# Optimization experiments

Measured on AMD Instinct MI355X. Metric: run time of the kernel, lower is better.

## Reference

```python
import jax, jax.numpy as jnp
import numpy as np

Q_MAX = 127.0  # int8 symmetric quant range
EPS = 1e-7

def setup_inputs() -> dict:
    key = jax.random.key(0)
    k1, k2, k3, k4 = jax.random.split(key, 4)
    M, K, N = 8192, 4096, 4096
    x = jax.random.normal(k1, (M, K), dtype=jnp.float32)
    # int8 weight stored as int32 for portability; values in [-127, 127]
    weight_i8 = jax.random.randint(k2, (N, K), -127, 128, dtype=jnp.int32)
    # per-output-channel weight scale (small positive)
    w_scale = jax.random.uniform(k3, (N,), dtype=jnp.float32) * 0.01 + 1e-4
    bias = jax.random.normal(k4, (N,), dtype=jnp.float32)
    return {"x": x, "weight_i8": weight_i8, "w_scale": w_scale, "bias": bias}

def reference(x, weight_i8, w_scale, bias):
    # per-token dynamic symmetric quantization of activations
    absmax = jnp.max(jnp.abs(x), axis=-1, keepdims=True)            # [M, 1]
    x_scale = jnp.maximum(absmax, EPS) / Q_MAX                       # [M, 1]
    x_q = jnp.clip(jnp.round(x / x_scale), -Q_MAX, Q_MAX)            # [M, K] int values in fp32
    acc = jnp.einsum('mk,nk->mn', x_q, weight_i8.astype(jnp.float32))  # [M, N]
    out = acc * x_scale * w_scale[None, :] + bias[None, :]
    return out
```

## Files before the change

### kernel.cpp

```cpp
#include <hip/hip_runtime.h>
#include <stdint.h>

#define Q_MAX_F 127.0f
#define EPS_F 1e-7f

typedef int   v4i __attribute__((ext_vector_type(4)));
typedef float v4f __attribute__((ext_vector_type(4)));

__global__ __launch_bounds__(256) void quant_x_kernel(
    const float* __restrict__ x, int8_t* __restrict__ xq,
    float* __restrict__ xscale, int K) {
  const int row = blockIdx.x;
  const int t = threadIdx.x;
  const float* xr = x + (size_t)row * K;

  float v[16];
  float m = 0.f;
#pragma unroll
  for (int c = 0; c < 4; ++c) {
    v4f f = *(const v4f*)(xr + c * 1024 + t * 4);
#pragma unroll
    for (int j = 0; j < 4; ++j) {
      v[c * 4 + j] = f[j];
      m = fmaxf(m, fabsf(f[j]));
    }
  }
#pragma unroll
  for (int off = 32; off; off >>= 1) m = fmaxf(m, __shfl_xor(m, off));
  __shared__ float sm[4];
  if ((t & 63) == 0) sm[t >> 6] = m;
  __syncthreads();
  m = fmaxf(fmaxf(sm[0], sm[1]), fmaxf(sm[2], sm[3]));

  const float s = fmaxf(m, EPS_F) / Q_MAX_F;
  const float inv = 1.0f / s;
  if (t == 0) xscale[row] = s;

  int* xqi = (int*)xq;
#pragma unroll
  for (int c = 0; c < 4; ++c) {
    int packed = 0;
#pragma unroll
    for (int j = 0; j < 4; ++j) {
      float q = rintf(v[c * 4 + j] * inv);
      q = fminf(fmaxf(q, -127.f), 127.f);
      packed |= ((int)q & 0xff) << (8 * j);
    }
    xqi[(size_t)row * (K / 4) + c * 256 + t] = packed;
  }
}

__global__ __launch_bounds__(256) void pack_w_kernel(
    const int* __restrict__ w, int8_t* __restrict__ wq, long n4) {
  long i = (long)blockIdx.x * 256 + threadIdx.x;
  if (i >= n4) return;
  v4i a = ((const v4i*)w)[i];
  int packed = (a[0] & 0xff) | ((a[1] & 0xff) << 8) |
               ((a[2] & 0xff) << 16) | ((a[3] & 0xff) << 24);
  ((int*)wq)[i] = packed;
}

#define BM 256
#define BN 256

__global__ __launch_bounds__(512, 2) void w8a8_gemm_kernel(
    const int8_t* __restrict__ xq, const int8_t* __restrict__ wq,
    const float* __restrict__ xscale, const float* __restrict__ wscale,
    const float* __restrict__ bias, float* __restrict__ out,
    int M, int N, int K) {
  extern __shared__ char lds[];

  const int t = threadIdx.x;
  const int lane = t & 63;
  const int wid = t >> 6;
  const int wr = wid >> 2;
  const int wc = wid & 3;

  const int nwg = gridDim.x;
  int bid = blockIdx.x;
  int wg = ((nwg & 7) == 0) ? ((bid & 7) * (nwg >> 3) + (bid >> 3)) : bid;

  const int nbn = N / BN;
  const int bm = (wg / nbn) * BM;
  const int bn = (wg % nbn) * BN;

  const char* gA = (const char*)xq + (size_t)bm * K;
  const char* gB = (const char*)wq + (size_t)bn * K;

  v4i acc[8][4] = {};

  auto stage_part = [&](int kt, int p) {
    const char* gsrc = p ? gB : gA;
    char* dstbase = lds + (size_t)(kt & 3) * 32768 + p * 16384;
#pragma unroll
    for (int i = 0; i < 2; ++i) {
      const int lin = i * 8192 + wid * 1024 + lane * 16;
      const int row = lin >> 6;
      const int cs = (lane & 3) ^ ((row >> 1) & 3);
      const char* src = gsrc + (size_t)row * K + kt * 64 + cs * 16;
      __builtin_amdgcn_global_load_lds(
          (const __attribute__((address_space(1))) void*)src,
          (__attribute__((address_space(3))) void*)(dstbase + i * 8192 + wid * 1024),
          16, 0, 0);
    }
  };

  const int NT = K / 64;
  const int rl = lane & 15;
  const int ck = lane >> 4;

  for (int kt = 0; kt < 3; ++kt) { stage_part(kt, 0); stage_part(kt, 1); }
  asm volatile("s_waitcnt vmcnt(8)" ::: "memory");
  asm volatile("s_barrier" ::: "memory");

  for (int kt = 0; kt < NT; ++kt) {
    const char* bufA = lds + (size_t)(kt & 3) * 32768;
    const char* bufB = bufA + 16384;

    v4i b[4], a[4];
#pragma unroll
    for (int j = 0; j < 4; ++j) {
      const int r = wc * 64 + j * 16 + rl;
      b[j] = *(const v4i*)(bufB + r * 64 + ((ck ^ ((r >> 1) & 3)) << 4));
    }
#pragma unroll
    for (int i = 0; i < 4; ++i) {
      const int r = wr * 128 + i * 16 + rl;
      a[i] = *(const v4i*)(bufA + r * 64 + ((ck ^ ((r >> 1) & 3)) << 4));
    }
    if (kt + 3 < NT) stage_part(kt + 3, 0);
    __builtin_amdgcn_s_setprio(1);
#pragma unroll
    for (int i = 0; i < 4; ++i)
#pragma unroll
      for (int j = 0; j < 4; ++j)
        acc[i][j] = __builtin_amdgcn_mfma_i32_16x16x64_i8(a[i], b[j], acc[i][j], 0, 0, 0);
    __builtin_amdgcn_s_setprio(0);
    asm volatile("s_barrier" ::: "memory");

#pragma unroll
    for (int i = 0; i < 4; ++i) {
      const int r = wr * 128 + 64 + i * 16 + rl;
      a[i] = *(const v4i*)(bufA + r * 64 + ((ck ^ ((r >> 1) & 3)) << 4));
    }
    if (kt + 3 < NT) stage_part(kt + 3, 1);
    __builtin_amdgcn_s_setprio(1);
#pragma unroll
    for (int i = 0; i < 4; ++i)
#pragma unroll
      for (int j = 0; j < 4; ++j)
        acc[4 + i][j] = __builtin_amdgcn_mfma_i32_16x16x64_i8(a[i], b[j], acc[4 + i][j], 0, 0, 0);
    __builtin_amdgcn_s_setprio(0);

    if (kt <= NT - 4)      asm volatile("s_waitcnt vmcnt(8)" ::: "memory");
    else if (kt == NT - 3) asm volatile("s_waitcnt vmcnt(4)" ::: "memory");
    else if (kt == NT - 2) asm volatile("s_waitcnt vmcnt(0)" ::: "memory");
    asm volatile("s_barrier" ::: "memory");
  }

  const int r0 = (lane >> 4) * 4;
  const int cn = lane & 15;
#pragma unroll
  for (int i = 0; i < 8; ++i) {
    const int growb = bm + wr * 128 + i * 16 + r0;
#pragma unroll
    for (int j = 0; j < 4; ++j) {
      const int gcol = bn + wc * 64 + j * 16 + cn;
      const float wsc = wscale[gcol];
      const float bs = bias[gcol];
#pragma unroll
      for (int r = 0; r < 4; ++r) {
        const int grow = growb + r;
        const float xs = xscale[grow];
        out[(size_t)grow * N + gcol] = (float)acc[i][j][r] * (xs * wsc) + bs;
      }
    }
  }
}

extern "C" void kernel_launch(void* const* d_in, const int* in_sizes, int n_in,
                              void* d_out, int out_size, void* d_ws, size_t ws_size,
                              hipStream_t stream) {
  const float* x = (const float*)d_in[0];
  const int* w = (const int*)d_in[1];
  const float* wscale = (const float*)d_in[2];
  const float* bias = (const float*)d_in[3];
  float* out = (float*)d_out;

  const int N = in_sizes[2];
  const long wk = (long)in_sizes[1];
  const int K = (int)(wk / N);
  const int M = (int)((long)in_sizes[0] / K);

  int8_t* xq = (int8_t*)d_ws;
  int8_t* wq = xq + (size_t)M * K;
  float* xscale = (float*)(wq + (size_t)N * K);

  quant_x_kernel<<<M, 256, 0, stream>>>(x, xq, xscale, K);

  const long n4 = (long)N * K / 4;
  pack_w_kernel<<<(int)((n4 + 255) / 256), 256, 0, stream>>>(w, wq, n4);

  const int nwg = (M / BM) * (N / BN);
  w8a8_gemm_kernel<<<nwg, 512, 131072, stream>>>(xq, wq, xscale, wscale, bias,
                                                 out, M, N, K);
}
```

Before: 398.7 us.

## Switch GEMM to 32x32x32 int8 MFMA and fuse quant/pack prep kernels

The GEMM inner loop moves from 16x16x64 to 32x32x32 int8 MFMA tiles. Both A and B stages are issued at the start of each k-step, and the mid-iteration barrier is dropped. The activation quantization and weight packing kernels are merged into one launch that splits its blocks between the two jobs with grid-stride loops, and each thread now writes one 16-byte vector per row. This aims to cut launch overhead, halve LDS fragment reads per MFMA and give larger MFMA ops, at the cost of a new epilogue layout and less overlap between LDS reads and staging.

```diff
diff --git a/kernel.cpp b/kernel.cpp
--- a/kernel.cpp
+++ b/kernel.cpp
@@ -4,60 +4,62 @@
 #define Q_MAX_F 127.0f
 #define EPS_F 1e-7f
 
-typedef int   v4i __attribute__((ext_vector_type(4)));
-typedef float v4f __attribute__((ext_vector_type(4)));
-
-__global__ __launch_bounds__(256) void quant_x_kernel(
+typedef int   v4i  __attribute__((ext_vector_type(4)));
+typedef int   v16i __attribute__((ext_vector_type(16)));
+typedef float v4f  __attribute__((ext_vector_type(4)));
+
+__global__ __launch_bounds__(256) void prep_kernel(
     const float* __restrict__ x, int8_t* __restrict__ xq,
-    float* __restrict__ xscale, int K) {
-  const int row = blockIdx.x;
+    float* __restrict__ xscale,
+    const int* __restrict__ w, int8_t* __restrict__ wq,
+    int M, int K, long n4, int QB) {
   const int t = threadIdx.x;
-  const float* xr = x + (size_t)row * K;
-
-  float v[16];
-  float m = 0.f;
-#pragma unroll
-  for (int c = 0; c < 4; ++c) {
-    v4f f = *(const v4f*)(xr + c * 1024 + t * 4);
-#pragma unroll
-    for (int j = 0; j < 4; ++j) {
-      v[c * 4 + j] = f[j];
-      m = fmaxf(m, fabsf(f[j]));
+  if ((int)blockIdx.x < QB) {
+    __shared__ float sm[4];
+    for (int row = blockIdx.x; row < M; row += QB) {
+      const float* xr = x + (size_t)row * K + t * 16;
+      float v[16];
+      float m = 0.f;
+#pragma unroll
+      for (int c = 0; c < 4; ++c) {
+        v4f f = *(const v4f*)(xr + c * 4);
+#pragma unroll
+        for (int j = 0; j < 4; ++j) {
+          v[c * 4 + j] = f[j];
+          m = fmaxf(m, fabsf(f[j]));
+        }
+      }
+#pragma unroll
+      for (int off = 32; off; off >>= 1) m = fmaxf(m, __shfl_xor(m, off));
+      if ((t & 63) == 0) sm[t >> 6] = m;
+      __syncthreads();
+      m = fmaxf(fmaxf(sm[0], sm[1]), fmaxf(sm[2], sm[3]));
+      __syncthreads();
+      const float s = fmaxf(m, EPS_F) / Q_MAX_F;
+      const float inv = 1.0f / s;
+      if (t == 0) xscale[row] = s;
+      v4i pk;
+#pragma unroll
+      for (int c = 0; c < 4; ++c) {
+        int pw = 0;
+#pragma unroll
+        for (int j = 0; j < 4; ++j) {
+          float q = rintf(v[c * 4 + j] * inv);
+          q = fminf(fmaxf(q, -127.f), 127.f);
+          pw |= ((int)q & 0xff) << (8 * j);
+        }
+        pk[c] = pw;
+      }
+      *(v4i*)(xq + (size_t)row * K + t * 16) = pk;
+    }
+  } else {
+    const long stride = (long)(gridDim.x - QB) * 256;
+    for (long i = (long)((int)blockIdx.x - QB) * 256 + t; i < n4; i += stride) {
+      v4i a = ((const v4i*)w)[i];
+      ((int*)wq)[i] = (a[0] & 0xff) | ((a[1] & 0xff) << 8) |
+                      ((a[2] & 0xff) << 16) | ((a[3] & 0xff) << 24);
     }
   }
-#pragma unroll
-  for (int off = 32; off; off >>= 1) m = fmaxf(m, __shfl_xor(m, off));
-  __shared__ float sm[4];
-  if ((t & 63) == 0) sm[t >> 6] = m;
-  __syncthreads();
-  m = fmaxf(fmaxf(sm[0], sm[1]), fmaxf(sm[2], sm[3]));
-
-  const float s = fmaxf(m, EPS_F) / Q_MAX_F;
-  const float inv = 1.0f / s;
-  if (t == 0) xscale[row] = s;
-
-  int* xqi = (int*)xq;
-#pragma unroll
-  for (int c = 0; c < 4; ++c) {
-    int packed = 0;
-#pragma unroll
-    for (int j = 0; j < 4; ++j) {
-      float q = rintf(v[c * 4 + j] * inv);
-      q = fminf(fmaxf(q, -127.f), 127.f);
-      packed |= ((int)q & 0xff) << (8 * j);
-    }
-    xqi[(size_t)row * (K / 4) + c * 256 + t] = packed;
-  }
-}
-
-__global__ __launch_bounds__(256) void pack_w_kernel(
-    const int* __restrict__ w, int8_t* __restrict__ wq, long n4) {
-  long i = (long)blockIdx.x * 256 + threadIdx.x;
-  if (i >= n4) return;
-  v4i a = ((const v4i*)w)[i];
-  int packed = (a[0] & 0xff) | ((a[1] & 0xff) << 8) |
-               ((a[2] & 0xff) << 16) | ((a[3] & 0xff) << 24);
-  ((int*)wq)[i] = packed;
 }
 
 #define BM 256
@@ -87,7 +89,7 @@
   const char* gA = (const char*)xq + (size_t)bm * K;
   const char* gB = (const char*)wq + (size_t)bn * K;
 
-  v4i acc[8][4] = {};
+  v16i acc[4][2] = {};
 
   auto stage_part = [&](int kt, int p) {
     const char* gsrc = p ? gB : gA;
@@ -106,8 +108,8 @@
   };
 
   const int NT = K / 64;
-  const int rl = lane & 15;
-  const int ck = lane >> 4;
+  const int cl = lane & 31;
+  const int ch = lane >> 5;
 
   for (int kt = 0; kt < 3; ++kt) { stage_part(kt, 0); stage_part(kt, 1); }
   asm volatile("s_waitcnt vmcnt(8)" ::: "memory");
@@ -117,39 +119,34 @@
     const char* bufA = lds + (size_t)(kt & 3) * 32768;
     const char* bufB = bufA + 16384;
 
-    v4i b[4], a[4];
-#pragma unroll
-    for (int j = 0; j < 4; ++j) {
-      const int r = wc * 64 + j * 16 + rl;
-      b[j] = *(const v4i*)(bufB + r * 64 + ((ck ^ ((r >> 1) & 3)) << 4));
-    }
-#pragma unroll
-    for (int i = 0; i < 4; ++i) {
-      const int r = wr * 128 + i * 16 + rl;
-      a[i] = *(const v4i*)(bufA + r * 64 + ((ck ^ ((r >> 1) & 3)) << 4));
-    }
-    if (kt + 3 < NT) stage_part(kt + 3, 0);
+    if (kt + 3 < NT) { stage_part(kt + 3, 0); stage_part(kt + 3, 1); }
+
+    v4i a[2][4], b[2][2];
+#pragma unroll
+    for (int ks = 0; ks < 2; ++ks) {
+#pragma unroll
+      for (int fi = 0; fi < 4; ++fi) {
+        const int r = wr * 128 + fi * 32 + cl;
+        const int c = (ch + 2 * ks) ^ ((r >> 1) & 3);
+        a[ks][fi] = *(const v4i*)(bufA + r * 64 + (c << 4));
+      }
+#pragma unroll
+      for (int fj = 0; fj < 2; ++fj) {
+        const int r = wc * 64 + fj * 32 + cl;
+        const int c = (ch + 2 * ks) ^ ((r >> 1) & 3);
+        b[ks][fj] = *(const v4i*)(bufB + r * 64 + (c << 4));
+      }
+    }
+
     __builtin_amdgcn_s_setprio(1);
 #pragma unroll
-    for (int i = 0; i < 4; ++i)
-#pragma unroll
-      for (int j = 0; j < 4; ++j)
-        acc[i][j] = __builtin_amdgcn_mfma_i32_16x16x64_i8(a[i], b[j], acc[i][j], 0, 0, 0);
-    __builtin_amdgcn_s_setprio(0);
-    asm volatile("s_barrier" ::: "memory");
-
-#pragma unroll
-    for (int i = 0; i < 4; ++i) {
-      const int r = wr * 128 + 64 + i * 16 + rl;
-      a[i] = *(const v4i*)(bufA + r * 64 + ((ck ^ ((r >> 1) & 3)) << 4));
-    }
-    if (kt + 3 < NT) stage_part(kt + 3, 1);
-    __builtin_amdgcn_s_setprio(1);
-#pragma unroll
-    for (int i = 0; i < 4; ++i)
-#pragma unroll
-      for (int j = 0; j < 4; ++j)
-        acc[4 + i][j] = __builtin_amdgcn_mfma_i32_16x16x64_i8(a[i], b[j], acc[4 + i][j], 0, 0, 0);
+    for (int ks = 0; ks < 2; ++ks)
+#pragma unroll
+      for (int fi = 0; fi < 4; ++fi)
+#pragma unroll
+        for (int fj = 0; fj < 2; ++fj)
+          acc[fi][fj] = __builtin_amdgcn_mfma_i32_32x32x32_i8(
+              a[ks][fi], b[ks][fj], acc[fi][fj], 0, 0, 0);
     __builtin_amdgcn_s_setprio(0);
 
     if (kt <= NT - 4)      asm volatile("s_waitcnt vmcnt(8)" ::: "memory");
@@ -158,22 +155,20 @@
     asm volatile("s_barrier" ::: "memory");
   }
 
-  const int r0 = (lane >> 4) * 4;
-  const int cn = lane & 15;
-#pragma unroll
-  for (int i = 0; i < 8; ++i) {
-    const int growb = bm + wr * 128 + i * 16 + r0;
-#pragma unroll
-    for (int j = 0; j < 4; ++j) {
-      const int gcol = bn + wc * 64 + j * 16 + cn;
-      const float wsc = wscale[gcol];
-      const float bs = bias[gcol];
-#pragma unroll
-      for (int r = 0; r < 4; ++r) {
-        const int grow = growb + r;
-        const float xs = xscale[grow];
-        out[(size_t)grow * N + gcol] = (float)acc[i][j][r] * (xs * wsc) + bs;
-      }
+  const int hl = lane >> 5;
+  const float wsc0 = wscale[bn + wc * 64 + cl];
+  const float wsc1 = wscale[bn + wc * 64 + 32 + cl];
+  const float bs0 = bias[bn + wc * 64 + cl];
+  const float bs1 = bias[bn + wc * 64 + 32 + cl];
+#pragma unroll
+  for (int fi = 0; fi < 4; ++fi) {
+#pragma unroll
+    for (int r = 0; r < 16; ++r) {
+      const int grow = bm + wr * 128 + fi * 32 + (r & 3) + 8 * (r >> 2) + 4 * hl;
+      const float xs = xscale[grow];
+      float* orow = out + (size_t)grow * N + bn + wc * 64 + cl;
+      orow[0]  = (float)acc[fi][0][r] * (xs * wsc0) + bs0;
+      orow[32] = (float)acc[fi][1][r] * (xs * wsc1) + bs1;
     }
   }
 }
@@ -196,10 +191,9 @@
   int8_t* wq = xq + (size_t)M * K;
   float* xscale = (float*)(wq + (size_t)N * K);
 
-  quant_x_kernel<<<M, 256, 0, stream>>>(x, xq, xscale, K);
-
   const long n4 = (long)N * K / 4;
-  pack_w_kernel<<<(int)((n4 + 255) / 256), 256, 0, stream>>>(w, wq, n4);
+  const int QB = 2048, PB = 2048;
+  prep_kernel<<<QB + PB, 256, 0, stream>>>(x, xq, xscale, w, wq, M, K, n4, QB);
 
   const int nwg = (M / BM) * (N / BN);
   w8a8_gemm_kernel<<<nwg, 512, 131072, stream>>>(xq, wq, xscale, wscale, bias,
```

Measured after the change: 415.2 us. 1.04x slower.
